# Kernel tuning notes

Measured on AMD Instinct MI355X. Metric: run time of the kernel, lower is better.

Reference implementation:

```python
import jax, jax.numpy as jnp
import numpy as np

B, W, N = 4, 8, 1024
F_IN, HID, OUT = 256, 256, 128


def setup_inputs() -> dict:
    key = jax.random.key(0)
    ks = jax.random.split(key, 8)
    X = jax.random.normal(ks[0], (B, W, N, F_IN), dtype=jnp.float32)
    adj = jax.random.uniform(ks[1], (B, W, N, N), dtype=jnp.float32)
    # Linear params, torch default init: U(-1/sqrt(fan_in), 1/sqrt(fan_in))
    def lin(k, fi, fo):
        k1, k2 = jax.random.split(k)
        bnd = 1.0 / np.sqrt(fi)
        Wm = jax.random.uniform(k1, (fi, fo), minval=-bnd, maxval=bnd, dtype=jnp.float32)
        bm = jax.random.uniform(k2, (fo,), minval=-bnd, maxval=bnd, dtype=jnp.float32)
        return Wm, bm
    W1, b1 = lin(ks[2], F_IN, HID)
    W2, b2 = lin(ks[3], HID, HID)
    W3, b3 = lin(ks[4], HID, OUT)
    return {"X": X, "adj": adj, "W1": W1, "b1": b1, "W2": W2, "b2": b2, "W3": W3, "b3": b3}


def _normalize(adj):
    # adj: [B, W, N, N]. adj_hat = adj + I; sym degree norm D^-1/2 A D^-1/2
    n = adj.shape[-1]
    adj_hat = adj + jnp.eye(n, dtype=adj.dtype)
    d = jnp.sum(adj_hat, axis=-1) ** (-0.5)            # [B, W, N]
    # diag(d) @ adj_hat @ diag(d) == row/col scaling (same math, no N^3 diag matmuls)
    return adj_hat * d[..., :, None] * d[..., None, :]


def reference(X, adj, W1, b1, W2, b2, W3, b3):
    adj_norm = _normalize(adj)                          # [B, W, N, N]
    h = X
    for Wm, bm in ((W1, b1), (W2, b2), (W3, b3)):
        h = jnp.einsum('bwnm,bwmf->bwnf', adj_norm, h)  # aggregate
        h = jax.nn.relu(jnp.einsum('bwnf,fo->bwno', h, Wm) + bm)
    return h                                            # [B, W, N, OUT]
```

## Files before the change

kernel.cpp:

```cpp
#include <hip/hip_runtime.h>
#include <hip/hip_bf16.h>
#include <cstdint>
#include <cstddef>

#define NN 1024
#define FF 256

typedef __attribute__((ext_vector_type(8))) short bf16x8;
typedef __attribute__((ext_vector_type(4))) float f32x4;

typedef __attribute__((address_space(1))) const void* gas_ptr;
typedef __attribute__((address_space(3))) void* las_ptr;

__device__ __forceinline__ short f2bf(float x) {
  unsigned int u = __float_as_uint(x);
  u = (u + 0x7fffu + ((u >> 16) & 1u)) >> 16;
  return (short)u;
}


__global__ __launch_bounds__(256)
void dinv_cast(const float* __restrict__ adj, float* __restrict__ dinv,
               short* __restrict__ Ahat) {
  __shared__ float wsum[64];
  int b = blockIdx.x;
  int bw = b >> 6, s = b & 63;
  int t = threadIdx.x;
  int wid = t >> 6, lane = t & 63;
  int row = lane & 15;
  int rloc = (s << 4) + row;
  int kg = (lane >> 4) & 3;
  const float* arow = adj + ((size_t)(bw << 10) + rloc) * NN;
  short* outb = Ahat + ((size_t)bw << 20) + ((size_t)s << 14) + (t << 3);
  float ssum = 0.f;
  #pragma unroll
  for (int it = 0; it < 8; it++) {
    int col = (it << 7) + (wid << 5) + (kg << 3);
    float4 a0 = *(const float4*)(arow + col);
    float4 a1 = *(const float4*)(arow + col + 4);
    float v[8] = {a0.x, a0.y, a0.z, a0.w, a1.x, a1.y, a1.z, a1.w};
    union { ushort o[8]; int4 q; } pk;
    #pragma unroll
    for (int j = 0; j < 8; j++) {
      v[j] += (rloc == col + j) ? 1.f : 0.f;
      ssum += v[j];
      pk.o[j] = (ushort)f2bf(v[j]);
    }
    *(int4*)(outb + (it << 11)) = pk.q;
  }
  ssum += __shfl_down(ssum, 32, 64);
  ssum += __shfl_down(ssum, 16, 64);
  if (lane < 16) wsum[(wid << 4) + lane] = ssum;
  __syncthreads();
  if (t < 16) {
    float tot = wsum[t] + wsum[16 + t] + wsum[32 + t] + wsum[48 + t];
    dinv[(bw << 10) + (s << 4) + t] = rsqrtf(tot);
  }
}

__global__ __launch_bounds__(256)
void preproc_xw(const float* __restrict__ X, const float* __restrict__ dinv,
                short* __restrict__ XT,
                const float* __restrict__ W1, const float* __restrict__ W2,
                const float* __restrict__ W3,
                short* __restrict__ T1, short* __restrict__ T2,
                short* __restrict__ T3) {
  __shared__ short T[64][72];
  int b = blockIdx.x;
  int t = threadIdx.x;
  if (b < 2048) {
    int bwo = b >> 6;
    int n0 = (b & 15) << 6, f0 = ((b >> 4) & 3) << 6;
    {
      int n = t >> 2, fc = (t & 3) << 4;
      float dn = dinv[(bwo << 10) + n0 + n];
      const float* src = X + (((size_t)bwo * NN + n0 + n) * FF) + f0 + fc;
      #pragma unroll
      for (int i = 0; i < 4; i++) {
        float4 v = ((const float4*)src)[i];
        ushort4 p;
        p.x = (unsigned short)f2bf(v.x * dn); p.y = (unsigned short)f2bf(v.y * dn);
        p.z = (unsigned short)f2bf(v.z * dn); p.w = (unsigned short)f2bf(v.w * dn);
        *(ushort4*)&T[n][fc + (i << 2)] = p;
      }
    }
    __syncthreads();
    {
      int f = t >> 2, nc = (t & 3) << 4;
      int fg = f0 + f, ng = n0 + nc;
      short tmp[16];
      #pragma unroll
      for (int i = 0; i < 16; i++) tmp[i] = T[nc + i][f];
      size_t e0 = ((size_t)bwo << 18) + ((size_t)(fg >> 4) << 14) + ((ng >> 5) << 9)
                + (((ng & 31) >> 3) << 7) + ((fg & 15) << 3);
      *(int4*)(XT + e0)       = *(int4*)&tmp[0];
      *(int4*)(XT + e0 + 128) = *(int4*)&tmp[8];
    }
  } else {
    int idx = (b - 2048) * 256 + t;
    const float* W; short* Td; int FO; int loc;
    if (idx < 65536)       { W = W1; Td = T1; FO = 256; loc = idx; }
    else if (idx < 131072) { W = W2; Td = T2; FO = 256; loc = idx - 65536; }
    else                   { W = W3; Td = T3; FO = 128; loc = idx - 131072; }
    int fo = loc >> 8, fi = loc & 255;
    if (fo < FO) {
      size_t e = (size_t)((fo >> 4) << 12) + ((fi >> 5) << 9)
               + (((fi & 31) >> 3) << 7) + ((fo & 15) << 3) + (fi & 7);
      Td[e] = f2bf(W[fi * FO + fo]);
    }
  }
}

template<int F_OUT, bool FINAL>
__global__ __launch_bounds__(512)
void gcn_layer(const short* __restrict__ Ahat,
               const float* __restrict__ dinv,
               const short* __restrict__ Gin,
               const short* __restrict__ WT,
               const float* __restrict__ bias,
               short* __restrict__ Gout,
               float* __restrict__ Out) {
  __shared__ __align__(16) short lds[34816];

  int b = blockIdx.x;
  int x = b & 7, m = b >> 3;
  int bw = (x << 2) + (m >> 3);
  int rb = m & 7;
  int r0 = rb << 7;

  int tid = threadIdx.x;
  int wid = tid >> 6, lane = tid & 63;
  int l15 = lane & 15, l4 = lane >> 4;
  int wr = wid >> 2, wf = wid & 3;

  const float* dvB = dinv + (bw << 10);
  const short* Hb = Gin + ((size_t)bw << 18) + ((size_t)(wf << 2) << 14) + (lane << 3);
  const short* Abase = Ahat + ((size_t)bw << 20) + ((size_t)(rb << 3) << 14);

  auto stageA = [&](int sel, int t) {
    char* base = (char*)lds + (sel << 14);
    #pragma unroll
    for (int i = 0; i < 2; i++) {
      int slot = (i << 9) + tid;
      int c = slot >> 6, o = slot & 63;
      const short* g = Abase + ((size_t)(c >> 1) << 14)
                     + ((size_t)((t << 1) + (c & 1)) << 9) + (o << 3);
      __builtin_amdgcn_global_load_lds((gas_ptr)g, (las_ptr)(base + (slot << 4)), 16, 0, 0);
    }
  };

  f32x4 acc[4][4];
  #pragma unroll
  for (int ah = 0; ah < 4; ah++)
    #pragma unroll
    for (int aa = 0; aa < 4; aa++) acc[ah][aa] = f32x4{0.f, 0.f, 0.f, 0.f};

  bf16x8 hE[4][2], hO[4][2];

#define LOADH(HB, T)                                                          \
  { _Pragma("unroll")                                                         \
    for (int ah = 0; ah < 4; ah++) {                                          \
      HB[ah][0] = *(const bf16x8*)(Hb + ah * 16384 + (size_t)(2 * (T)) * 512);\
      HB[ah][1] = *(const bf16x8*)(Hb + ah * 16384 + (size_t)(2 * (T) + 1) * 512); } }

#define DSREADA(AB, PAR)                                                      \
  { const char* ab_ = (const char*)lds + ((PAR) << 14);                       \
    _Pragma("unroll")                                                         \
    for (int aa = 0; aa < 4; aa++) {                                          \
      int c_ = ((wr << 2) + aa) << 1;                                         \
      AB[aa][0] = *(const bf16x8*)(ab_ + (c_ << 10) + (lane << 4));           \
      AB[aa][1] = *(const bf16x8*)(ab_ + ((c_ + 1) << 10) + (lane << 4)); } }

#define MM(HB, AB)                                                            \
  __builtin_amdgcn_s_setprio(1);                                              \
  _Pragma("unroll")                                                           \
  for (int kt = 0; kt < 2; kt++)                                              \
    _Pragma("unroll")                                                         \
    for (int ah = 0; ah < 4; ah++)                                            \
      _Pragma("unroll")                                                       \
      for (int aa = 0; aa < 4; aa++)                                          \
        acc[ah][aa] = __builtin_amdgcn_mfma_f32_16x16x32_bf16(                \
            HB[ah][kt], AB[aa][kt], acc[ah][aa], 0, 0, 0);                    \
  __builtin_amdgcn_s_setprio(0);

  stageA(0, 0);
  __builtin_amdgcn_sched_barrier(0);
  LOADH(hE, 0);
  asm volatile("s_waitcnt vmcnt(8)" ::: "memory");
  __builtin_amdgcn_sched_barrier(0);
  __builtin_amdgcn_s_barrier();

  #pragma unroll
  for (int it = 0; it < 8; ++it) {
    const int t0 = 2 * it, t1 = t0 + 1;
    if (t0 < 15) stageA(1, t1);
    __builtin_amdgcn_sched_barrier(0);
    if (t0 < 15) LOADH(hO, t1);
    {
      bf16x8 aF[4][2];
      DSREADA(aF, 0);
      MM(hE, aF);
    }
    if (t0 < 15) { asm volatile("s_waitcnt vmcnt(8)" ::: "memory"); }
    else         { asm volatile("s_waitcnt vmcnt(0)" ::: "memory"); }
    __builtin_amdgcn_sched_barrier(0);
    __builtin_amdgcn_s_barrier();
    if (t1 > 15) break;
    if (t1 < 15) stageA(0, t1 + 1);
    __builtin_amdgcn_sched_barrier(0);
    if (t1 < 15) LOADH(hE, t1 + 1);
    {
      bf16x8 aG[4][2];
      DSREADA(aG, 1);
      MM(hO, aG);
    }
    if (t1 < 15) { asm volatile("s_waitcnt vmcnt(8)" ::: "memory"); }
    else         { asm volatile("s_waitcnt vmcnt(0)" ::: "memory"); }
    __builtin_amdgcn_sched_barrier(0);
    __builtin_amdgcn_s_barrier();
  }
#undef LOADH
#undef DSREADA
#undef MM

  short* aggL = lds;
  float dsc[4];
  #pragma unroll
  for (int aa = 0; aa < 4; aa++) dsc[aa] = dvB[r0 + (wr << 6) + (aa << 4) + l15];
  #pragma unroll
  for (int ah = 0; ah < 4; ah++)
    #pragma unroll
    for (int aa = 0; aa < 4; aa++) {
      int r = (wr << 6) + (aa << 4) + l15;
      int fB = ((wf << 6) + (ah << 4) + (l4 << 2)) << 1;
      int off = (r * 544 + (fB ^ ((r & 7) << 4))) >> 1;
      ushort4 p;
      p.x = (unsigned short)f2bf(acc[ah][aa][0] * dsc[aa]);
      p.y = (unsigned short)f2bf(acc[ah][aa][1] * dsc[aa]);
      p.z = (unsigned short)f2bf(acc[ah][aa][2] * dsc[aa]);
      p.w = (unsigned short)f2bf(acc[ah][aa][3] * dsc[aa]);
      *(ushort4*)(aggL + off) = p;
    }
  __syncthreads();

  constexpr int NFO = F_OUT / 64;
  const short* Wbase = WT + (size_t)(wf * NFO) * 4096 + (lane << 3);
  f32x4 acc2[4][NFO];
  #pragma unroll
  for (int am = 0; am < 4; am++)
    #pragma unroll
    for (int nf = 0; nf < NFO; nf++) acc2[am][nf] = f32x4{0.f, 0.f, 0.f, 0.f};

  #pragma unroll
  for (int kt = 0; kt < 8; kt++) {
    bf16x8 af[4];
    #pragma unroll
    for (int am = 0; am < 4; am++) {
      int r = (wr << 6) + (am << 4) + l15;
      int fB = (kt << 6) + (l4 << 4);
      af[am] = *(const bf16x8*)(aggL + ((r * 544 + (fB ^ ((r & 7) << 4))) >> 1));
    }
    #pragma unroll
    for (int nf = 0; nf < NFO; nf++) {
      bf16x8 wv = *(const bf16x8*)(Wbase + (size_t)nf * 4096 + (kt << 9));
      #pragma unroll
      for (int am = 0; am < 4; am++)
        acc2[am][nf] = __builtin_amdgcn_mfma_f32_16x16x32_bf16(af[am], wv, acc2[am][nf], 0, 0, 0);
    }
  }

  #pragma unroll
  for (int am = 0; am < 4; am++) {
    int nodeLoc = (wr << 6) + (am << 4) + (l4 << 2);
    float4 dn4 = *(const float4*)(dvB + r0 + nodeLoc);
    float dn[4] = {dn4.x, dn4.y, dn4.z, dn4.w};
    #pragma unroll
    for (int nf = 0; nf < NFO; nf++) {
      int fo = wf * (F_OUT / 4) + (nf << 4) + l15;
      float bb = bias[fo];
      float v[4];
      #pragma unroll
      for (int j = 0; j < 4; j++) v[j] = fmaxf(acc2[am][nf][j] + bb, 0.f);
      if (!FINAL) {
        ushort4 p;
        p.x = (unsigned short)f2bf(v[0] * dn[0]);
        p.y = (unsigned short)f2bf(v[1] * dn[1]);
        p.z = (unsigned short)f2bf(v[2] * dn[2]);
        p.w = (unsigned short)f2bf(v[3] * dn[3]);
        size_t e = (size_t)bw * (F_OUT * 1024) + ((size_t)(fo >> 4) << 14)
                 + ((size_t)((rb << 2) + (wr << 1) + (am >> 1)) << 9)
                 + ((size_t)(((am & 1) << 1) + (l4 >> 1)) << 7)
                 + ((fo & 15) << 3) + ((l4 & 1) << 2);
        *(ushort4*)(Gout + e) = p;
      } else {
        float* ob = Out + ((size_t)(bw << 10) + r0 + nodeLoc) * F_OUT + fo;
        ob[0]         = v[0];
        ob[F_OUT]     = v[1];
        ob[2 * F_OUT] = v[2];
        ob[3 * F_OUT] = v[3];
      }
    }
  }
}

extern "C" void kernel_launch(void* const* d_in, const int* in_sizes, int n_in,
                              void* d_out, int out_size, void* d_ws, size_t ws_size,
                              hipStream_t stream) {
  const float* X   = (const float*)d_in[0];
  const float* adj = (const float*)d_in[1];
  const float* W1  = (const float*)d_in[2];
  const float* b1  = (const float*)d_in[3];
  const float* W2  = (const float*)d_in[4];
  const float* b2  = (const float*)d_in[5];
  const float* W3  = (const float*)d_in[6];
  const float* b3  = (const float*)d_in[7];
  float* out = (float*)d_out;

  char* ws = (char*)d_ws;
  float* dinv = (float*)ws;
  short* WT1  = (short*)(ws + 131072);
  short* WT2  = (short*)(ws + 262144);
  short* WT3  = (short*)(ws + 393216);
  short* bufA = (short*)(ws + 458752);
  short* bufB = (short*)(ws + 458752 + 16777216);
  short* Ahat = (short*)(ws + 458752 + 2 * 16777216);

  dinv_cast<<<2048, 256, 0, stream>>>(adj, dinv, Ahat);
  preproc_xw<<<2688, 256, 0, stream>>>(X, dinv, bufA, W1, W2, W3, WT1, WT2, WT3);

  gcn_layer<256, false><<<256, 512, 0, stream>>>(Ahat, dinv, bufA, WT1, b1, bufB, nullptr);
  gcn_layer<256, false><<<256, 512, 0, stream>>>(Ahat, dinv, bufB, WT2, b2, bufA, nullptr);
  gcn_layer<128, true ><<<256, 512, 0, stream>>>(Ahat, dinv, bufA, WT3, b3, nullptr, out);
}
```

Before: 135.4 us.

## Halve waves per GCN layer block, giving each wave all 128 rows

Reduces the gcn_layer block from 8 waves to 4, so each wave covers all 128 node rows of the tile for its 64-feature slice instead of 64 rows. H fragments loaded from global memory are now reused across twice as many A tiles, cutting redundant global H loads, and the aggregation and weight-GEMM accumulators double per wave. In exchange the kernel loses wave-level parallelism within each block and has much higher register pressure (128 accumulator VGPRs just for aggregation), which could cause spills or worse latency hiding with only 256 blocks.

```diff
diff --git a/kernel.cpp b/kernel.cpp
--- a/kernel.cpp
+++ b/kernel.cpp
@@ -112,7 +112,7 @@
 }
 
 template<int F_OUT, bool FINAL>
-__global__ __launch_bounds__(512)
+__global__ __launch_bounds__(256, 1)
 void gcn_layer(const short* __restrict__ Ahat,
                const float* __restrict__ dinv,
                const short* __restrict__ Gin,
@@ -129,9 +129,8 @@
   int r0 = rb << 7;
 
   int tid = threadIdx.x;
-  int wid = tid >> 6, lane = tid & 63;
+  int wf = tid >> 6, lane = tid & 63;
   int l15 = lane & 15, l4 = lane >> 4;
-  int wr = wid >> 2, wf = wid & 3;
 
   const float* dvB = dinv + (bw << 10);
   const short* Hb = Gin + ((size_t)bw << 18) + ((size_t)(wf << 2) << 14) + (lane << 3);
@@ -140,8 +139,8 @@
   auto stageA = [&](int sel, int t) {
     char* base = (char*)lds + (sel << 14);
     #pragma unroll
-    for (int i = 0; i < 2; i++) {
-      int slot = (i << 9) + tid;
+    for (int i = 0; i < 4; i++) {
+      int slot = (i << 8) + tid;
       int c = slot >> 6, o = slot & 63;
       const short* g = Abase + ((size_t)(c >> 1) << 14)
                      + ((size_t)((t << 1) + (c & 1)) << 9) + (o << 3);
@@ -149,11 +148,11 @@
     }
   };
 
-  f32x4 acc[4][4];
+  f32x4 acc[4][8];
   #pragma unroll
   for (int ah = 0; ah < 4; ah++)
     #pragma unroll
-    for (int aa = 0; aa < 4; aa++) acc[ah][aa] = f32x4{0.f, 0.f, 0.f, 0.f};
+    for (int aa = 0; aa < 8; aa++) acc[ah][aa] = f32x4{0.f, 0.f, 0.f, 0.f};
 
   bf16x8 hE[4][2], hO[4][2];
 
@@ -163,25 +162,25 @@
       HB[ah][0] = *(const bf16x8*)(Hb + ah * 16384 + (size_t)(2 * (T)) * 512);\
       HB[ah][1] = *(const bf16x8*)(Hb + ah * 16384 + (size_t)(2 * (T) + 1) * 512); } }
 
-#define DSREADA(AB, PAR)                                                      \
+#define MMHALF(HB, PAR, AA0)                                                  \
   { const char* ab_ = (const char*)lds + ((PAR) << 14);                       \
+    bf16x8 aT[4][2];                                                          \
     _Pragma("unroll")                                                         \
-    for (int aa = 0; aa < 4; aa++) {                                          \
-      int c_ = ((wr << 2) + aa) << 1;                                         \
-      AB[aa][0] = *(const bf16x8*)(ab_ + (c_ << 10) + (lane << 4));           \
-      AB[aa][1] = *(const bf16x8*)(ab_ + ((c_ + 1) << 10) + (lane << 4)); } }
-
-#define MM(HB, AB)                                                            \
-  __builtin_amdgcn_s_setprio(1);                                              \
-  _Pragma("unroll")                                                           \
-  for (int kt = 0; kt < 2; kt++)                                              \
+    for (int q = 0; q < 4; q++) {                                             \
+      int c_ = (((AA0) + q) << 1);                                            \
+      aT[q][0] = *(const bf16x8*)(ab_ + (c_ << 10) + (lane << 4));            \
+      aT[q][1] = *(const bf16x8*)(ab_ + ((c_ + 1) << 10) + (lane << 4));      \
+    }                                                                         \
+    __builtin_amdgcn_s_setprio(1);                                            \
     _Pragma("unroll")                                                         \
-    for (int ah = 0; ah < 4; ah++)                                            \
+    for (int kt = 0; kt < 2; kt++)                                            \
       _Pragma("unroll")                                                       \
-      for (int aa = 0; aa < 4; aa++)                                          \
-        acc[ah][aa] = __builtin_amdgcn_mfma_f32_16x16x32_bf16(                \
-            HB[ah][kt], AB[aa][kt], acc[ah][aa], 0, 0, 0);                    \
-  __builtin_amdgcn_s_setprio(0);
+      for (int ah = 0; ah < 4; ah++)                                          \
+        _Pragma("unroll")                                                     \
+        for (int q = 0; q < 4; q++)                                           \
+          acc[ah][(AA0) + q] = __builtin_amdgcn_mfma_f32_16x16x32_bf16(       \
+              HB[ah][kt], aT[q][kt], acc[ah][(AA0) + q], 0, 0, 0);            \
+    __builtin_amdgcn_s_setprio(0); }
 
   stageA(0, 0);
   __builtin_amdgcn_sched_barrier(0);
@@ -196,11 +195,8 @@
     if (t0 < 15) stageA(1, t1);
     __builtin_amdgcn_sched_barrier(0);
     if (t0 < 15) LOADH(hO, t1);
-    {
-      bf16x8 aF[4][2];
-      DSREADA(aF, 0);
-      MM(hE, aF);
-    }
+    MMHALF(hE, 0, 0);
+    MMHALF(hE, 0, 4);
     if (t0 < 15) { asm volatile("s_waitcnt vmcnt(8)" ::: "memory"); }
     else         { asm volatile("s_waitcnt vmcnt(0)" ::: "memory"); }
     __builtin_amdgcn_sched_barrier(0);
@@ -209,29 +205,25 @@
     if (t1 < 15) stageA(0, t1 + 1);
     __builtin_amdgcn_sched_barrier(0);
     if (t1 < 15) LOADH(hE, t1 + 1);
-    {
-      bf16x8 aG[4][2];
-      DSREADA(aG, 1);
-      MM(hO, aG);
-    }
+    MMHALF(hO, 1, 0);
+    MMHALF(hO, 1, 4);
     if (t1 < 15) { asm volatile("s_waitcnt vmcnt(8)" ::: "memory"); }
     else         { asm volatile("s_waitcnt vmcnt(0)" ::: "memory"); }
     __builtin_amdgcn_sched_barrier(0);
     __builtin_amdgcn_s_barrier();
   }
 #undef LOADH
-#undef DSREADA
-#undef MM
+#undef MMHALF
 
   short* aggL = lds;
-  float dsc[4];
-  #pragma unroll
-  for (int aa = 0; aa < 4; aa++) dsc[aa] = dvB[r0 + (wr << 6) + (aa << 4) + l15];
+  float dsc[8];
+  #pragma unroll
+  for (int aa = 0; aa < 8; aa++) dsc[aa] = dvB[r0 + (aa << 4) + l15];
   #pragma unroll
   for (int ah = 0; ah < 4; ah++)
     #pragma unroll
-    for (int aa = 0; aa < 4; aa++) {
-      int r = (wr << 6) + (aa << 4) + l15;
+    for (int aa = 0; aa < 8; aa++) {
+      int r = (aa << 4) + l15;
       int fB = ((wf << 6) + (ah << 4) + (l4 << 2)) << 1;
       int off = (r * 544 + (fB ^ ((r & 7) << 4))) >> 1;
       ushort4 p;
@@ -245,18 +237,18 @@
 
   constexpr int NFO = F_OUT / 64;
   const short* Wbase = WT + (size_t)(wf * NFO) * 4096 + (lane << 3);
-  f32x4 acc2[4][NFO];
-  #pragma unroll
-  for (int am = 0; am < 4; am++)
+  f32x4 acc2[8][NFO];
+  #pragma unroll
+  for (int am = 0; am < 8; am++)
     #pragma unroll
     for (int nf = 0; nf < NFO; nf++) acc2[am][nf] = f32x4{0.f, 0.f, 0.f, 0.f};
 
   #pragma unroll
   for (int kt = 0; kt < 8; kt++) {
-    bf16x8 af[4];
-    #pragma unroll
-    for (int am = 0; am < 4; am++) {
-      int r = (wr << 6) + (am << 4) + l15;
+    bf16x8 af[8];
+    #pragma unroll
+    for (int am = 0; am < 8; am++) {
+      int r = (am << 4) + l15;
       int fB = (kt << 6) + (l4 << 4);
       af[am] = *(const bf16x8*)(aggL + ((r * 544 + (fB ^ ((r & 7) << 4))) >> 1));
     }
@@ -264,14 +256,14 @@
     for (int nf = 0; nf < NFO; nf++) {
       bf16x8 wv = *(const bf16x8*)(Wbase + (size_t)nf * 4096 + (kt << 9));
       #pragma unroll
-      for (int am = 0; am < 4; am++)
+      for (int am = 0; am < 8; am++)
         acc2[am][nf] = __builtin_amdgcn_mfma_f32_16x16x32_bf16(af[am], wv, acc2[am][nf], 0, 0, 0);
     }
   }
 
   #pragma unroll
-  for (int am = 0; am < 4; am++) {
-    int nodeLoc = (wr << 6) + (am << 4) + (l4 << 2);
+  for (int am = 0; am < 8; am++) {
+    int nodeLoc = (am << 4) + (l4 << 2);
     float4 dn4 = *(const float4*)(dvB + r0 + nodeLoc);
     float dn[4] = {dn4.x, dn4.y, dn4.z, dn4.w};
     #pragma unroll
@@ -288,7 +280,7 @@
         p.z = (unsigned short)f2bf(v[2] * dn[2]);
         p.w = (unsigned short)f2bf(v[3] * dn[3]);
         size_t e = (size_t)bw * (F_OUT * 1024) + ((size_t)(fo >> 4) << 14)
-                 + ((size_t)((rb << 2) + (wr << 1) + (am >> 1)) << 9)
+                 + ((size_t)((rb << 2) + (am >> 1)) << 9)
                  + ((size_t)(((am & 1) << 1) + (l4 >> 1)) << 7)
                  + ((fo & 15) << 3) + ((l4 & 1) << 2);
         *(ushort4*)(Gout + e) = p;
@@ -328,7 +320,7 @@
   dinv_cast<<<2048, 256, 0, stream>>>(adj, dinv, Ahat);
   preproc_xw<<<2688, 256, 0, stream>>>(X, dinv, bufA, W1, W2, W3, WT1, WT2, WT3);
 
-  gcn_layer<256, false><<<256, 512, 0, stream>>>(Ahat, dinv, bufA, WT1, b1, bufB, nullptr);
-  gcn_layer<256, false><<<256, 512, 0, stream>>>(Ahat, dinv, bufB, WT2, b2, bufA, nullptr);
-  gcn_layer<128, true ><<<256, 512, 0, stream>>>(Ahat, dinv, bufA, WT3, b3, nullptr, out);
-}
+  gcn_layer<256, false><<<256, 256, 0, stream>>>(Ahat, dinv, bufA, WT1, b1, bufB, nullptr);
+  gcn_layer<256, false><<<256, 256, 0, stream>>>(Ahat, dinv, bufB, WT2, b2, bufA, nullptr);
+  gcn_layer<128, true ><<<256, 256, 0, stream>>>(Ahat, dinv, bufA, WT3, b3, nullptr, out);
+}
```

After: 137.1 us. Within noise of the previous version (+1.2%).
